# Performance work log

Measured on AMD Instinct MI355X. Metric: run time of the kernel, lower is better.

## Reference

```python
import jax, jax.numpy as jnp
import numpy as np

B, S, D, H, FF = 2, 2048, 1024, 16, 4096
DK = D // H
EPS = 1e-6  # LayerNormalization eps


def setup_inputs() -> dict:
    key = jax.random.key(0)
    ks = jax.random.split(key, 12)
    n = lambda k, shp, s=0.02: (jax.random.normal(k, shp, jnp.float32) * s)
    z = lambda shp: jnp.zeros(shp, jnp.float32)
    return {
        "x": jax.random.normal(ks[0], (B, S, D), jnp.float32),
        # attention projections (torch Linear: weight [out, in], bias [out])
        "wq": n(ks[1], (D, D)), "bq": z((D,)),
        "wk": n(ks[2], (D, D)), "bk": z((D,)),
        "wv": n(ks[3], (D, D)), "bv": z((D,)),
        "wo": n(ks[4], (D, D)), "bo": z((D,)),
        # feed-forward
        "w1": n(ks[5], (FF, D)), "b1": z((FF,)),
        "w2": n(ks[6], (D, FF)), "b2": z((D,)),
        # custom LayerNormalization: scalar alpha (ones(1)) and bias (zeros(1))
        "ln1_a": jnp.ones((1,), jnp.float32), "ln1_b": z((1,)),
        "ln2_a": jnp.ones((1,), jnp.float32), "ln2_b": z((1,)),
        # original code path uses `if mask:` -> falsy None; represented as 0
        "src_mask": 0,
    }


def _layernorm(x, alpha, bias):
    # Faithful to source: alpha * (x - mean) / sqrt(std + eps) + bias,
    # with std the UNBIASED std (torch default) and sqrt applied to std itself.
    mean = jnp.mean(x, axis=-1, keepdims=True)
    std = jnp.std(x, axis=-1, keepdims=True, ddof=1)
    return alpha * (x - mean) / jnp.sqrt(std + EPS) + bias


def _mha(x, wq, bq, wk, bk, wv, bv, wo, bo):
    # x: (B, S, D)
    q = (jnp.einsum("bsd,ed->bse", x, wq) + bq).reshape(B, S, H, DK).transpose(0, 2, 1, 3)
    k = (jnp.einsum("bsd,ed->bse", x, wk) + bk).reshape(B, S, H, DK).transpose(0, 2, 1, 3)
    v = (jnp.einsum("bsd,ed->bse", x, wv) + bv).reshape(B, S, H, DK).transpose(0, 2, 1, 3)
    scores = jnp.einsum("bhqd,bhkd->bhqk", q, k) / jnp.sqrt(jnp.float32(DK))
    attn = jax.nn.softmax(scores, axis=-1)  # mask is None, dropout eval -> identity
    out = jnp.einsum("bhqk,bhkd->bhqd", attn, v)
    out = out.transpose(0, 2, 1, 3).reshape(B, S, D)
    return jnp.einsum("bsd,ed->bse", out, wo) + bo


def reference(x, wq, bq, wk, bk, wv, bv, wo, bo, w1, b1, w2, b2,
              ln1_a, ln1_b, ln2_a, ln2_b, src_mask):
    # residual 1: pre-norm self-attention
    h = x + _mha(_layernorm(x, ln1_a, ln1_b), wq, bq, wk, bk, wv, bv, wo, bo)
    # residual 2: pre-norm FFN (linear -> relu -> linear)
    hn = _layernorm(h, ln2_a, ln2_b)
    ffn = jnp.einsum("bsf,df->bsd", jax.nn.relu(jnp.einsum("bsd,fd->bsf", hn, w1) + b1), w2) + b2
    return h + ffn
```

## Files before the change

kernel.cpp:

```cpp
#include <hip/hip_runtime.h>
#include <stdint.h>

#define Bb 2
#define Ss 2048
#define Dd 1024
#define Hh 16
#define DKk 64
#define FFf 4096
#define Mm 4096
#define LN_EPS 1e-6f
#define QB 64
#define KVB 64

typedef __attribute__((ext_vector_type(8))) short bf16x8;
typedef __attribute__((ext_vector_type(4))) float f32x4;

#define GLOAD_LDS(gptr, lptr) \
  __builtin_amdgcn_global_load_lds((const __attribute__((address_space(1))) void*)(gptr), \
                                   (__attribute__((address_space(3))) void*)(lptr), 16, 0, 0)

__device__ __forceinline__ unsigned short f32_to_bf16(float f) {
  union { float f; uint32_t u; } v; v.f = f;
  uint32_t u = v.u;
  u += 0x7FFFu + ((u >> 16) & 1u);
  return (unsigned short)(u >> 16);
}

struct CastArgs {
  const float4* src[6];
  ushort4* dst[6];
  int cum[7];
};
__global__ __launch_bounds__(256) void cast_all(CastArgs a, int total4) {
  int stride = gridDim.x * blockDim.x;
  for (int i = blockIdx.x * blockDim.x + threadIdx.x; i < total4; i += stride) {
    int s = 0;
    #pragma unroll
    for (int k = 1; k < 6; ++k) s += (i >= a.cum[k]);
    float4 v = a.src[s][i - a.cum[s]];
    ushort4 o;
    o.x = f32_to_bf16(v.x); o.y = f32_to_bf16(v.y);
    o.z = f32_to_bf16(v.z); o.w = f32_to_bf16(v.w);
    a.dst[s][i - a.cum[s]] = o;
  }
}

__global__ __launch_bounds__(256) void layernorm_kernel(
    const float* __restrict__ x, const float* __restrict__ alpha_p,
    const float* __restrict__ bias_p, unsigned short* __restrict__ out)
{
  __shared__ float redS[4], redQ[4];
  int row = blockIdx.x, tid = threadIdx.x;
  const float4 v = ((const float4*)(x + (size_t)row * Dd))[tid];
  float s  = v.x + v.y + v.z + v.w;
  float sq = v.x*v.x + v.y*v.y + v.z*v.z + v.w*v.w;
  #pragma unroll
  for (int off = 32; off; off >>= 1) { s += __shfl_down(s, off); sq += __shfl_down(sq, off); }
  if ((tid & 63) == 0) { redS[tid >> 6] = s; redQ[tid >> 6] = sq; }
  __syncthreads();
  float S  = redS[0] + redS[1] + redS[2] + redS[3];
  float Qq = redQ[0] + redQ[1] + redQ[2] + redQ[3];
  float mean = S * (1.f / Dd);
  float var  = fmaxf((Qq - mean * S) * (1.f / (Dd - 1)), 0.f);
  float k    = alpha_p[0] / sqrtf(sqrtf(var) + LN_EPS);
  float bias = bias_p[0];
  ushort4 ov;
  ov.x = f32_to_bf16((v.x - mean) * k + bias);
  ov.y = f32_to_bf16((v.y - mean) * k + bias);
  ov.z = f32_to_bf16((v.z - mean) * k + bias);
  ov.w = f32_to_bf16((v.w - mean) * k + bias);
  ((ushort4*)(out + (size_t)row * Dd))[tid] = ov;
}

template<int FLAGS>
__global__ __launch_bounds__(256) void gemm_bt(
    const unsigned short* __restrict__ A,
    const unsigned short* __restrict__ W,
    const float* __restrict__ bias,
    const float* __restrict__ resid,
    void* __restrict__ Cout,
    int M, int N, int K)
{
  __shared__ unsigned short As[2][128 * 32];
  __shared__ unsigned short Bs[2][128 * 32];
  const int tid  = threadIdx.x;
  const int lane = tid & 63;
  const int wid  = tid >> 6;
  const int wr   = wid >> 1, wc = wid & 1;
  const int brow = blockIdx.y * 128;
  const int bcol = blockIdx.x * 128;
  const int lane15 = lane & 15;
  const int laneK8 = (lane >> 4) * 8;

  f32x4 acc[4][4] = {};

  auto STAGE = [&](int kk2, int bufi) {
    #pragma unroll
    for (int rnd = 0; rnd < 2; ++rnd) {
      int f   = rnd * 4096 + tid * 16;
      int row = f >> 6;
      int ce  = (f & 63) >> 1;
      GLOAD_LDS(A + (size_t)(brow + row) * K + kk2 + ce, &As[bufi][rnd * 2048 + wid * 512]);
      GLOAD_LDS(W + (size_t)(bcol + row) * K + kk2 + ce, &Bs[bufi][rnd * 2048 + wid * 512]);
    }
  };

  STAGE(0, 0);
  __syncthreads();
  int cur = 0;
  for (int kk = 0; kk < K; kk += 32) {
    if (kk + 32 < K) STAGE(kk + 32, cur ^ 1);

    bf16x8 af[4], bfr[4];
    #pragma unroll
    for (int i = 0; i < 4; ++i) {
      af[i]  = *(const bf16x8*)&As[cur][(wr * 64 + i * 16 + lane15) * 32 + laneK8];
      bfr[i] = *(const bf16x8*)&Bs[cur][(wc * 64 + i * 16 + lane15) * 32 + laneK8];
    }
    #pragma unroll
    for (int i = 0; i < 4; ++i)
      #pragma unroll
      for (int j = 0; j < 4; ++j)
        acc[i][j] = __builtin_amdgcn_mfma_f32_16x16x32_bf16(af[i], bfr[j], acc[i][j], 0, 0, 0);
    __syncthreads();
    cur ^= 1;
  }

  #pragma unroll
  for (int i = 0; i < 4; ++i) {
    int row0 = brow + wr * 64 + i * 16 + (lane >> 4) * 4;
    #pragma unroll
    for (int j = 0; j < 4; ++j) {
      int col = bcol + wc * 64 + j * 16 + lane15;
      float bv = bias[col];
      #pragma unroll
      for (int r = 0; r < 4; ++r) {
        float v = acc[i][j][r] + bv;
        if (FLAGS & 1) v = fmaxf(v, 0.f);
        size_t idx = (size_t)(row0 + r) * N + col;
        if (FLAGS & 2) ((float*)Cout)[idx] = resid[idx] + v;
        else           ((unsigned short*)Cout)[idx] = f32_to_bf16(v);
      }
    }
  }
}

template<int FLAGS>
__global__ __launch_bounds__(256) void gemm_bt64(
    const unsigned short* __restrict__ A,
    const unsigned short* __restrict__ W,
    const float* __restrict__ bias,
    const float* __restrict__ resid,
    void* __restrict__ Cout,
    int M, int N, int K)
{
  __shared__ unsigned short As[2][64 * 64];
  __shared__ unsigned short Bs[2][128 * 64];
  const int tid  = threadIdx.x;
  const int lane = tid & 63;
  const int wid  = tid >> 6;
  const int wr   = wid >> 1, wc = wid & 1;
  const int brow = blockIdx.y * 64;
  const int bcol = blockIdx.x * 128;
  const int lane15 = lane & 15;
  const int lgb16  = (lane >> 4) * 16;

  f32x4 acc[2][4] = {};

  auto STAGE = [&](int kk2, int bufi) {
    #pragma unroll
    for (int rnd = 0; rnd < 2; ++rnd) {
      int p    = rnd * 4096 + tid * 16;
      int row  = p >> 7;
      int colu = ((p & 127) ^ ((row & 7) << 4)) >> 1;
      GLOAD_LDS(A + (size_t)(brow + row) * K + kk2 + colu, &As[bufi][rnd * 2048 + wid * 512]);
    }
    #pragma unroll
    for (int rnd = 0; rnd < 4; ++rnd) {
      int p    = rnd * 4096 + tid * 16;
      int row  = p >> 7;
      int colu = ((p & 127) ^ ((row & 7) << 4)) >> 1;
      GLOAD_LDS(W + (size_t)(bcol + row) * K + kk2 + colu, &Bs[bufi][rnd * 2048 + wid * 512]);
    }
  };

  STAGE(0, 0);
  __syncthreads();
  int cur = 0;
  for (int kk = 0; kk < K; kk += 64) {
    if (kk + 64 < K) STAGE(kk + 64, cur ^ 1);

    #pragma unroll
    for (int z = 0; z < 2; ++z) {
      bf16x8 af[2], bfr[4];
      #pragma unroll
      for (int i = 0; i < 2; ++i) {
        int r = wr * 32 + i * 16 + lane15;
        af[i] = *(const bf16x8*)((const char*)&As[cur][0] + (r << 7) + ((z * 64 + lgb16) ^ ((r & 7) << 4)));
      }
      #pragma unroll
      for (int j = 0; j < 4; ++j) {
        int r = wc * 64 + j * 16 + lane15;
        bfr[j] = *(const bf16x8*)((const char*)&Bs[cur][0] + (r << 7) + ((z * 64 + lgb16) ^ ((r & 7) << 4)));
      }
      #pragma unroll
      for (int i = 0; i < 2; ++i)
        #pragma unroll
        for (int j = 0; j < 4; ++j)
          acc[i][j] = __builtin_amdgcn_mfma_f32_16x16x32_bf16(af[i], bfr[j], acc[i][j], 0, 0, 0);
    }
    __syncthreads();
    cur ^= 1;
  }

  #pragma unroll
  for (int i = 0; i < 2; ++i) {
    int row0 = brow + wr * 32 + i * 16 + (lane >> 4) * 4;
    #pragma unroll
    for (int j = 0; j < 4; ++j) {
      int col = bcol + wc * 64 + j * 16 + lane15;
      float bv = bias[col];
      #pragma unroll
      for (int r = 0; r < 4; ++r) {
        float v = acc[i][j][r] + bv;
        if (FLAGS & 1) v = fmaxf(v, 0.f);
        size_t idx = (size_t)(row0 + r) * N + col;
        if (FLAGS & 2) ((float*)Cout)[idx] = resid[idx] + v;
        else           ((unsigned short*)Cout)[idx] = f32_to_bf16(v);
      }
    }
  }
}

__global__ __launch_bounds__(256) void gemm_qkv(
    const unsigned short* __restrict__ A,
    const unsigned short* __restrict__ W,
    const float* __restrict__ bq, const float* __restrict__ bk, const float* __restrict__ bv,
    unsigned short* __restrict__ Qb, unsigned short* __restrict__ Kb,
    unsigned short* __restrict__ Vt)
{
  const int K = Dd;
  __shared__ unsigned short As[2][128 * 32];
  __shared__ unsigned short Bs[2][128 * 32];
  const int tid  = threadIdx.x;
  const int lane = tid & 63;
  const int wid  = tid >> 6;
  const int wr   = wid >> 1, wc = wid & 1;
  const int brow = blockIdx.y * 128;
  const int bcol = blockIdx.x * 128;
  const int lane15 = lane & 15;
  const int laneK8 = (lane >> 4) * 8;

  f32x4 acc[4][4] = {};

  auto STAGE = [&](int kk2, int bufi) {
    #pragma unroll
    for (int rnd = 0; rnd < 2; ++rnd) {
      int f   = rnd * 4096 + tid * 16;
      int row = f >> 6;
      int ce  = (f & 63) >> 1;
      GLOAD_LDS(A + (size_t)(brow + row) * K + kk2 + ce, &As[bufi][rnd * 2048 + wid * 512]);
      GLOAD_LDS(W + (size_t)(bcol + row) * K + kk2 + ce, &Bs[bufi][rnd * 2048 + wid * 512]);
    }
  };

  STAGE(0, 0);
  __syncthreads();
  int cur = 0;
  for (int kk = 0; kk < K; kk += 32) {
    if (kk + 32 < K) STAGE(kk + 32, cur ^ 1);

    bf16x8 af[4], bfr[4];
    #pragma unroll
    for (int i = 0; i < 4; ++i) {
      af[i]  = *(const bf16x8*)&As[cur][(wr * 64 + i * 16 + lane15) * 32 + laneK8];
      bfr[i] = *(const bf16x8*)&Bs[cur][(wc * 64 + i * 16 + lane15) * 32 + laneK8];
    }
    #pragma unroll
    for (int i = 0; i < 4; ++i)
      #pragma unroll
      for (int j = 0; j < 4; ++j)
        acc[i][j] = __builtin_amdgcn_mfma_f32_16x16x32_bf16(af[i], bfr[j], acc[i][j], 0, 0, 0);
    __syncthreads();
    cur ^= 1;
  }

  const int region = bcol >> 10;
  const float* bp = (region == 0) ? bq : (region == 1) ? bk : bv;

  #pragma unroll
  for (int i = 0; i < 4; ++i) {
    int row0 = brow + wr * 64 + i * 16 + (lane >> 4) * 4;
    #pragma unroll
    for (int j = 0; j < 4; ++j) {
      int col = bcol + wc * 64 + j * 16 + lane15;
      int cl  = col & 1023;
      float bvv = bp[cl];
      if (region < 2) {
        unsigned short* dst = (region == 0) ? Qb : Kb;
        #pragma unroll
        for (int r = 0; r < 4; ++r)
          dst[(size_t)(row0 + r) * Dd + cl] = f32_to_bf16(acc[i][j][r] + bvv);
      } else {
        ushort4 pk;
        pk.x = f32_to_bf16(acc[i][j][0] + bvv);
        pk.y = f32_to_bf16(acc[i][j][1] + bvv);
        pk.z = f32_to_bf16(acc[i][j][2] + bvv);
        pk.w = f32_to_bf16(acc[i][j][3] + bvv);
        int bidx = row0 >> 11;
        int s0   = row0 & (Ss - 1);
        *(ushort4*)(Vt + ((size_t)(bidx * Dd + cl)) * Ss + s0) = pk;
      }
    }
  }
}

__global__ __launch_bounds__(256) void attn_mfma(
    const unsigned short* __restrict__ Q,
    const unsigned short* __restrict__ K,
    const unsigned short* __restrict__ Vt,
    unsigned short* __restrict__ ctx)
{
  __shared__ unsigned short Ks[2][KVB * 64];
  __shared__ unsigned short Vs[2][64 * KVB];
  __shared__ unsigned short Ps[4][16 * 64];

  const int tid  = threadIdx.x;
  const int lane = tid & 63;
  const int wid  = tid >> 6;
  const int l15  = lane & 15;
  const int lg   = lane >> 4;
  const int b    = blockIdx.y >> 4, h = blockIdx.y & 15;
  const int q0   = blockIdx.x * QB + wid * 16;

  const size_t qkbase = (size_t)b * Ss * Dd + (size_t)h * DKk;
  const size_t vtbase = ((size_t)b * Dd + h * DKk) * (size_t)Ss;
  const float KLOG = 0.125f * 1.44269504f;

  bf16x8 qf[2];
  #pragma unroll
  for (int z = 0; z < 2; ++z)
    qf[z] = *(const bf16x8*)(Q + qkbase + (size_t)(q0 + l15) * Dd + z * 32 + lg * 8);

  f32x4 acc_o[4] = {};
  float lrow[4] = {0.f, 0.f, 0.f, 0.f};

  auto STAGE = [&](int kt2, int bufi) {
    #pragma unroll
    for (int rnd = 0; rnd < 2; ++rnd) {
      int p    = rnd * 4096 + tid * 16;
      int row  = p >> 7;
      int colu = ((p & 127) ^ ((row & 7) << 4)) >> 1;
      GLOAD_LDS(K  + qkbase + (size_t)(kt2 + row) * Dd + colu, &Ks[bufi][rnd * 2048 + wid * 512]);
      GLOAD_LDS(Vt + vtbase + (size_t)row * Ss + kt2 + colu,   &Vs[bufi][rnd * 2048 + wid * 512]);
    }
  };

  STAGE(0, 0);
  __syncthreads();
  int cur = 0;

  for (int kt = 0; kt < Ss; kt += KVB) {
    if (kt + KVB < Ss) STAGE(kt + KVB, cur ^ 1);

    f32x4 accs[4] = {};
    const char* kb = (const char*)&Ks[cur][0];
    __builtin_amdgcn_s_setprio(1);
    #pragma unroll
    for (int cf = 0; cf < 4; ++cf) {
      int r = cf * 16 + l15;
      int rsw = (r & 7) << 4;
      #pragma unroll
      for (int z = 0; z < 2; ++z) {
        const bf16x8 kf = *(const bf16x8*)(kb + (r << 7) + ((z * 64 + lg * 16) ^ rsw));
        accs[cf] = __builtin_amdgcn_mfma_f32_16x16x32_bf16(qf[z], kf, accs[cf], 0, 0, 0);
      }
    }
    __builtin_amdgcn_s_setprio(0);

    #pragma unroll
    for (int ri = 0; ri < 4; ++ri) {
      float pv[4];
      #pragma unroll
      for (int cf = 0; cf < 4; ++cf)
        pv[cf] = __builtin_amdgcn_exp2f(accs[cf][ri] * KLOG);
      lrow[ri] += (pv[0] + pv[1]) + (pv[2] + pv[3]);
      int prow = lg * 4 + ri;
      int psw  = (prow & 7) << 4;
      char* pb = (char*)&Ps[wid][0] + (prow << 7);
      #pragma unroll
      for (int cf = 0; cf < 4; ++cf)
        *(unsigned short*)(pb + ((cf * 32 + l15 * 2) ^ psw)) =
            (unsigned short)(__float_as_uint(pv[cf]) >> 16);
    }

    const char* vb = (const char*)&Vs[cur][0];
    __builtin_amdgcn_s_setprio(1);
    #pragma unroll
    for (int kc = 0; kc < 2; ++kc) {
      int r = l15;
      const bf16x8 pf = *(const bf16x8*)((const char*)&Ps[wid][0] + (r << 7) + ((kc * 64 + lg * 16) ^ ((r & 7) << 4)));
      #pragma unroll
      for (int cf = 0; cf < 4; ++cf) {
        int vr = cf * 16 + l15;
        const bf16x8 vf = *(const bf16x8*)(vb + (vr << 7) + ((kc * 64 + lg * 16) ^ ((vr & 7) << 4)));
        acc_o[cf] = __builtin_amdgcn_mfma_f32_16x16x32_bf16(pf, vf, acc_o[cf], 0, 0, 0);
      }
    }
    __builtin_amdgcn_s_setprio(0);
    __syncthreads();
    cur ^= 1;
  }

  #pragma unroll
  for (int ri = 0; ri < 4; ++ri) {
    float l = lrow[ri];
    l += __shfl_xor(l, 1);
    l += __shfl_xor(l, 2);
    l += __shfl_xor(l, 4);
    l += __shfl_xor(l, 8);
    float inv = 1.f / l;
    int q = q0 + lg * 4 + ri;
    #pragma unroll
    for (int cf = 0; cf < 4; ++cf)
      ctx[qkbase + (size_t)q * Dd + cf * 16 + l15] = f32_to_bf16(acc_o[cf][ri] * inv);
  }
}

extern "C" void kernel_launch(void* const* d_in, const int* in_sizes, int n_in,
                              void* d_out, int out_size, void* d_ws, size_t ws_size,
                              hipStream_t stream)
{
  const float* x    = (const float*)d_in[0];
  const float* wq   = (const float*)d_in[1];
  const float* bq   = (const float*)d_in[2];
  const float* wk   = (const float*)d_in[3];
  const float* bk   = (const float*)d_in[4];
  const float* wv   = (const float*)d_in[5];
  const float* bv   = (const float*)d_in[6];
  const float* wo   = (const float*)d_in[7];
  const float* bo   = (const float*)d_in[8];
  const float* w1   = (const float*)d_in[9];
  const float* b1   = (const float*)d_in[10];
  const float* w2   = (const float*)d_in[11];
  const float* b2   = (const float*)d_in[12];
  const float* ln1a = (const float*)d_in[13];
  const float* ln1b = (const float*)d_in[14];
  const float* ln2a = (const float*)d_in[15];
  const float* ln2b = (const float*)d_in[16];

  char* ws = (char*)d_ws;
  const size_t MB = 1u << 20;
  unsigned short* wqkv_b = (unsigned short*)(ws + 0 * MB);
  unsigned short* wo_b   = (unsigned short*)(ws + 6 * MB);
  unsigned short* w1_b   = (unsigned short*)(ws + 8 * MB);
  unsigned short* w2_b   = (unsigned short*)(ws + 16 * MB);
  unsigned short* xn1    = (unsigned short*)(ws + 24 * MB);
  unsigned short* Qb     = (unsigned short*)(ws + 32 * MB);
  unsigned short* Kb     = (unsigned short*)(ws + 40 * MB);
  unsigned short* Vt     = (unsigned short*)(ws + 48 * MB);
  unsigned short* ctx    = (unsigned short*)(ws + 56 * MB);
  float*          h      = (float*)(ws + 64 * MB);
  unsigned short* hn2    = (unsigned short*)(ws + 80 * MB);
  unsigned short* f1     = (unsigned short*)(ws + 88 * MB);
  float* out = (float*)d_out;

  {
    const int DD4 = (Dd * Dd) >> 2;
    const int FD4 = (FFf * Dd) >> 2;
    CastArgs a;
    a.src[0] = (const float4*)wq; a.src[1] = (const float4*)wk; a.src[2] = (const float4*)wv;
    a.src[3] = (const float4*)wo; a.src[4] = (const float4*)w1; a.src[5] = (const float4*)w2;
    a.dst[0] = (ushort4*)wqkv_b;
    a.dst[1] = (ushort4*)(wqkv_b + 1 * Dd * Dd);
    a.dst[2] = (ushort4*)(wqkv_b + 2 * Dd * Dd);
    a.dst[3] = (ushort4*)wo_b;
    a.dst[4] = (ushort4*)w1_b;
    a.dst[5] = (ushort4*)w2_b;
    a.cum[0] = 0;
    a.cum[1] = DD4; a.cum[2] = 2 * DD4; a.cum[3] = 3 * DD4; a.cum[4] = 4 * DD4;
    a.cum[5] = 4 * DD4 + FD4; a.cum[6] = 4 * DD4 + 2 * FD4;
    cast_all<<<2048, 256, 0, stream>>>(a, a.cum[6]);
  }

  layernorm_kernel<<<Mm, 256, 0, stream>>>(x, ln1a, ln1b, xn1);
  gemm_qkv<<<dim3(3 * Dd / 128, Mm / 128), 256, 0, stream>>>(xn1, wqkv_b, bq, bk, bv, Qb, Kb, Vt);
  attn_mfma<<<dim3(Ss / QB, Bb * Hh), 256, 0, stream>>>(Qb, Kb, Vt, ctx);
  gemm_bt64<2><<<dim3(Dd / 128, Mm / 64), 256, 0, stream>>>(ctx, wo_b, bo, x, h, Mm, Dd, Dd);
  layernorm_kernel<<<Mm, 256, 0, stream>>>(h, ln2a, ln2b, hn2);
  gemm_bt<1><<<dim3(FFf / 128, Mm / 128), 256, 0, stream>>>(hn2, w1_b, b1, nullptr, f1, Mm, FFf, Dd);
  gemm_bt64<2><<<dim3(Dd / 128, Mm / 64), 256, 0, stream>>>(f1, w2_b, b2, h, out, Mm, Dd, FFf);
}
```

Measured before the change: 368.3 us.

## Replace QKV and FFN1 GEMMs with 256x256-tile 8-wave swizzled-LDS kernel

```diff
diff --git a/kernel.cpp b/kernel.cpp
--- a/kernel.cpp
+++ b/kernel.cpp
@@ -72,74 +72,116 @@
   ((ushort4*)(out + (size_t)row * Dd))[tid] = ov;
 }
 
-template<int FLAGS>
-__global__ __launch_bounds__(256) void gemm_bt(
+template<int MODE>
+__global__ __launch_bounds__(512) void gemm256(
     const unsigned short* __restrict__ A,
     const unsigned short* __restrict__ W,
-    const float* __restrict__ bias,
-    const float* __restrict__ resid,
-    void* __restrict__ Cout,
-    int M, int N, int K)
+    const float* __restrict__ b0, const float* __restrict__ b1, const float* __restrict__ b2,
+    void* __restrict__ o0, void* __restrict__ o1, void* __restrict__ o2,
+    int N, int K)
 {
-  __shared__ unsigned short As[2][128 * 32];
-  __shared__ unsigned short Bs[2][128 * 32];
+  __shared__ unsigned short As[2][256 * 64];
+  __shared__ unsigned short Bs[2][256 * 64];
   const int tid  = threadIdx.x;
   const int lane = tid & 63;
   const int wid  = tid >> 6;
-  const int wr   = wid >> 1, wc = wid & 1;
-  const int brow = blockIdx.y * 128;
-  const int bcol = blockIdx.x * 128;
-  const int lane15 = lane & 15;
-  const int laneK8 = (lane >> 4) * 8;
-
-  f32x4 acc[4][4] = {};
-
-  auto STAGE = [&](int kk2, int bufi) {
-    #pragma unroll
-    for (int rnd = 0; rnd < 2; ++rnd) {
-      int f   = rnd * 4096 + tid * 16;
-      int row = f >> 6;
-      int ce  = (f & 63) >> 1;
-      GLOAD_LDS(A + (size_t)(brow + row) * K + kk2 + ce, &As[bufi][rnd * 2048 + wid * 512]);
-      GLOAD_LDS(W + (size_t)(bcol + row) * K + kk2 + ce, &Bs[bufi][rnd * 2048 + wid * 512]);
+  const int wm   = wid >> 2;
+  const int wn   = wid & 3;
+  const int l15  = lane & 15;
+  const int lg   = lane >> 4;
+  const int brow = blockIdx.y * 256;
+  const int bcol = blockIdx.x * 256;
+  const int nt   = K >> 6;
+
+  f32x4 acc[8][4] = {};
+
+  auto STAGE4 = [&](int kk2, int bufi, int r0) {
+    #pragma unroll
+    for (int rr = 0; rr < 4; ++rr) {
+      const int r   = r0 + rr;
+      const int p   = (r & 3) * 8192 + tid * 16;
+      const int row = p >> 7;
+      const int cb  = (p & 127) ^ ((row & 7) << 4);
+      const unsigned short* g = (r < 4)
+          ? A + (size_t)(brow + row) * K + kk2 + (cb >> 1)
+          : W + (size_t)(bcol + row) * K + kk2 + (cb >> 1);
+      unsigned short* l = ((r < 4) ? &As[bufi][0] : &Bs[bufi][0]) + (r & 3) * 4096 + tid * 8;
+      GLOAD_LDS(g, l);
     }
   };
 
-  STAGE(0, 0);
+  STAGE4(0, 0, 0);
+  STAGE4(0, 0, 4);
   __syncthreads();
-  int cur = 0;
-  for (int kk = 0; kk < K; kk += 32) {
-    if (kk + 32 < K) STAGE(kk + 32, cur ^ 1);
-
-    bf16x8 af[4], bfr[4];
-    #pragma unroll
-    for (int i = 0; i < 4; ++i) {
-      af[i]  = *(const bf16x8*)&As[cur][(wr * 64 + i * 16 + lane15) * 32 + laneK8];
-      bfr[i] = *(const bf16x8*)&Bs[cur][(wc * 64 + i * 16 + lane15) * 32 + laneK8];
-    }
-    #pragma unroll
-    for (int i = 0; i < 4; ++i)
-      #pragma unroll
-      for (int j = 0; j < 4; ++j)
-        acc[i][j] = __builtin_amdgcn_mfma_f32_16x16x32_bf16(af[i], bfr[j], acc[i][j], 0, 0, 0);
-    __syncthreads();
-    cur ^= 1;
+
+  for (int t = 0; t < nt; ++t) {
+    const int cur = t & 1;
+    const char* Ab  = (const char*)&As[cur][0];
+    const char* Bbp = (const char*)&Bs[cur][0];
+    #pragma unroll
+    for (int ph = 0; ph < 4; ++ph) {
+      const int mq = ph & 1, ks = ph >> 1;
+      bf16x8 af[4], bfr[4];
+      #pragma unroll
+      for (int i = 0; i < 4; ++i) {
+        int row = wm * 128 + (mq * 4 + i) * 16 + l15;
+        af[i] = *(const bf16x8*)(Ab + (row << 7) + ((ks * 64 + lg * 16) ^ ((row & 7) << 4)));
+      }
+      #pragma unroll
+      for (int n = 0; n < 4; ++n) {
+        int row = wn * 64 + n * 16 + l15;
+        bfr[n] = *(const bf16x8*)(Bbp + (row << 7) + ((ks * 64 + lg * 16) ^ ((row & 7) << 4)));
+      }
+      if (ph < 2 && t + 1 < nt) STAGE4((t + 1) << 6, cur ^ 1, ph * 4);
+      __builtin_amdgcn_s_barrier();
+      asm volatile("s_waitcnt lgkmcnt(0)" ::: "memory");
+      __builtin_amdgcn_sched_barrier(0);
+      __builtin_amdgcn_s_setprio(1);
+      #pragma unroll
+      for (int i = 0; i < 4; ++i)
+        #pragma unroll
+        for (int n = 0; n < 4; ++n)
+          acc[mq * 4 + i][n] =
+              __builtin_amdgcn_mfma_f32_16x16x32_bf16(af[i], bfr[n], acc[mq * 4 + i][n], 0, 0, 0);
+      __builtin_amdgcn_s_setprio(0);
+      if (ph == 3) asm volatile("s_waitcnt vmcnt(0)" ::: "memory");
+      __builtin_amdgcn_s_barrier();
+      __builtin_amdgcn_sched_barrier(0);
+    }
   }
 
   #pragma unroll
-  for (int i = 0; i < 4; ++i) {
-    int row0 = brow + wr * 64 + i * 16 + (lane >> 4) * 4;
-    #pragma unroll
-    for (int j = 0; j < 4; ++j) {
-      int col = bcol + wc * 64 + j * 16 + lane15;
-      float bv = bias[col];
-      #pragma unroll
-      for (int r = 0; r < 4; ++r) {
-        float v = acc[i][j][r] + bv;
-        if (FLAGS & 1) v = fmaxf(v, 0.f);
-        size_t idx = (size_t)(row0 + r) * N + col;
-        if (FLAGS & 2) ((float*)Cout)[idx] = resid[idx] + v;
-        else           ((unsigned short*)Cout)[idx] = f32_to_bf16(v);
+  for (int m = 0; m < 8; ++m) {
+    int row0 = brow + wm * 128 + m * 16 + lg * 4;
+    #pragma unroll
+    for (int n = 0; n < 4; ++n) {
+      int col = bcol + wn * 64 + n * 16 + l15;
+      if (MODE == 0) {
+        float bv = b0[col];
+        #pragma unroll
+        for (int r = 0; r < 4; ++r)
+          ((unsigned short*)o0)[(size_t)(row0 + r) * N + col] =
+              f32_to_bf16(fmaxf(acc[m][n][r] + bv, 0.f));
+      } else {
+        const int region = bcol >> 10;
+        const int cl = col & 1023;
+        const float* bp = (region == 0) ? b0 : (region == 1) ? b1 : b2;
+        float bv = bp[cl];
+        if (region < 2) {
+          unsigned short* dst = (unsigned short*)((region == 0) ? o0 : o1);
+          #pragma unroll
+          for (int r = 0; r < 4; ++r)
+            dst[(size_t)(row0 + r) * Dd + cl] = f32_to_bf16(acc[m][n][r] + bv);
+        } else {
+          ushort4 pk;
+          pk.x = f32_to_bf16(acc[m][n][0] + bv);
+          pk.y = f32_to_bf16(acc[m][n][1] + bv);
+          pk.z = f32_to_bf16(acc[m][n][2] + bv);
+          pk.w = f32_to_bf16(acc[m][n][3] + bv);
+          int bidx = row0 >> 11;
+          int s0   = row0 & (Ss - 1);
+          *(ushort4*)((unsigned short*)o2 + ((size_t)(bidx * Dd + cl)) * Ss + s0) = pk;
+        }
       }
     }
   }
@@ -223,93 +265,9 @@
       #pragma unroll
       for (int r = 0; r < 4; ++r) {
         float v = acc[i][j][r] + bv;
-        if (FLAGS & 1) v = fmaxf(v, 0.f);
         size_t idx = (size_t)(row0 + r) * N + col;
         if (FLAGS & 2) ((float*)Cout)[idx] = resid[idx] + v;
         else           ((unsigned short*)Cout)[idx] = f32_to_bf16(v);
-      }
-    }
-  }
-}
-
-__global__ __launch_bounds__(256) void gemm_qkv(
-    const unsigned short* __restrict__ A,
-    const unsigned short* __restrict__ W,
-    const float* __restrict__ bq, const float* __restrict__ bk, const float* __restrict__ bv,
-    unsigned short* __restrict__ Qb, unsigned short* __restrict__ Kb,
-    unsigned short* __restrict__ Vt)
-{
-  const int K = Dd;
-  __shared__ unsigned short As[2][128 * 32];
-  __shared__ unsigned short Bs[2][128 * 32];
-  const int tid  = threadIdx.x;
-  const int lane = tid & 63;
-  const int wid  = tid >> 6;
-  const int wr   = wid >> 1, wc = wid & 1;
-  const int brow = blockIdx.y * 128;
-  const int bcol = blockIdx.x * 128;
-  const int lane15 = lane & 15;
-  const int laneK8 = (lane >> 4) * 8;
-
-  f32x4 acc[4][4] = {};
-
-  auto STAGE = [&](int kk2, int bufi) {
-    #pragma unroll
-    for (int rnd = 0; rnd < 2; ++rnd) {
-      int f   = rnd * 4096 + tid * 16;
-      int row = f >> 6;
-      int ce  = (f & 63) >> 1;
-      GLOAD_LDS(A + (size_t)(brow + row) * K + kk2 + ce, &As[bufi][rnd * 2048 + wid * 512]);
-      GLOAD_LDS(W + (size_t)(bcol + row) * K + kk2 + ce, &Bs[bufi][rnd * 2048 + wid * 512]);
-    }
-  };
-
-  STAGE(0, 0);
-  __syncthreads();
-  int cur = 0;
-  for (int kk = 0; kk < K; kk += 32) {
-    if (kk + 32 < K) STAGE(kk + 32, cur ^ 1);
-
-    bf16x8 af[4], bfr[4];
-    #pragma unroll
-    for (int i = 0; i < 4; ++i) {
-      af[i]  = *(const bf16x8*)&As[cur][(wr * 64 + i * 16 + lane15) * 32 + laneK8];
-      bfr[i] = *(const bf16x8*)&Bs[cur][(wc * 64 + i * 16 + lane15) * 32 + laneK8];
-    }
-    #pragma unroll
-    for (int i = 0; i < 4; ++i)
-      #pragma unroll
-      for (int j = 0; j < 4; ++j)
-        acc[i][j] = __builtin_amdgcn_mfma_f32_16x16x32_bf16(af[i], bfr[j], acc[i][j], 0, 0, 0);
-    __syncthreads();
-    cur ^= 1;
-  }
-
-  const int region = bcol >> 10;
-  const float* bp = (region == 0) ? bq : (region == 1) ? bk : bv;
-
-  #pragma unroll
-  for (int i = 0; i < 4; ++i) {
-    int row0 = brow + wr * 64 + i * 16 + (lane >> 4) * 4;
-    #pragma unroll
-    for (int j = 0; j < 4; ++j) {
-      int col = bcol + wc * 64 + j * 16 + lane15;
-      int cl  = col & 1023;
-      float bvv = bp[cl];
-      if (region < 2) {
-        unsigned short* dst = (region == 0) ? Qb : Kb;
-        #pragma unroll
-        for (int r = 0; r < 4; ++r)
-          dst[(size_t)(row0 + r) * Dd + cl] = f32_to_bf16(acc[i][j][r] + bvv);
-      } else {
-        ushort4 pk;
-        pk.x = f32_to_bf16(acc[i][j][0] + bvv);
-        pk.y = f32_to_bf16(acc[i][j][1] + bvv);
-        pk.z = f32_to_bf16(acc[i][j][2] + bvv);
-        pk.w = f32_to_bf16(acc[i][j][3] + bvv);
-        int bidx = row0 >> 11;
-        int s0   = row0 & (Ss - 1);
-        *(ushort4*)(Vt + ((size_t)(bidx * Dd + cl)) * Ss + s0) = pk;
       }
     }
   }
@@ -484,10 +442,12 @@
   }
 
   layernorm_kernel<<<Mm, 256, 0, stream>>>(x, ln1a, ln1b, xn1);
-  gemm_qkv<<<dim3(3 * Dd / 128, Mm / 128), 256, 0, stream>>>(xn1, wqkv_b, bq, bk, bv, Qb, Kb, Vt);
+  gemm256<1><<<dim3(3 * Dd / 256, Mm / 256), 512, 0, stream>>>(
+      xn1, wqkv_b, bq, bk, bv, Qb, Kb, Vt, 3 * Dd, Dd);
   attn_mfma<<<dim3(Ss / QB, Bb * Hh), 256, 0, stream>>>(Qb, Kb, Vt, ctx);
   gemm_bt64<2><<<dim3(Dd / 128, Mm / 64), 256, 0, stream>>>(ctx, wo_b, bo, x, h, Mm, Dd, Dd);
   layernorm_kernel<<<Mm, 256, 0, stream>>>(h, ln2a, ln2b, hn2);
-  gemm_bt<1><<<dim3(FFf / 128, Mm / 128), 256, 0, stream>>>(hn2, w1_b, b1, nullptr, f1, Mm, FFf, Dd);
+  gemm256<0><<<dim3(FFf / 256, Mm / 256), 512, 0, stream>>>(
+      hn2, w1_b, b1, nullptr, nullptr, f1, nullptr, nullptr, FFf, Dd);
   gemm_bt64<2><<<dim3(Dd / 128, Mm / 64), 256, 0, stream>>>(f1, w2_b, b2, h, out, Mm, Dd, FFf);
 }
```

Measured after the change: 353.9 us. 3.9% less time.
